# Kernel tuning notes

Measured on AMD Instinct MI355X. Metric: run time of the kernel, lower is better.

Reference implementation:

```python
import jax, jax.numpy as jnp
import numpy as np

NT, NGRID, NX, NY, H = 65536, 28, 19, 1, 20  # dims hard-coded by the torch module


def setup_inputs() -> dict:
    key = jax.random.key(0)
    ks = jax.random.split(key, 7)
    s = 1.0 / np.sqrt(H)  # torch default init scale for LSTMCell/Linear(20, ...)
    u = lambda k, shape: jax.random.uniform(k, shape, jnp.float32, -s, s)
    return {
        "x": jax.random.normal(ks[0], (NT, NGRID, NX), jnp.float32),
        "W_ih": u(ks[1], (4 * H, H)),   # LSTMCell weight_ih, input size 20 = nx + ny
        "W_hh": u(ks[2], (4 * H, H)),   # LSTMCell weight_hh
        "b_ih": u(ks[3], (4 * H,)),
        "b_hh": u(ks[4], (4 * H,)),
        "W_out": u(ks[5], (NY, H)),     # linearOut: Linear(20, ny)
        "b_out": u(ks[6], (NY,)),
    }


def reference(x, W_ih, W_hh, b_ih, b_hh, W_out, b_out):
    # x: (nt, ngrid, nx). Each step feeds concat(x_t, detach(prev_out)) -> LSTMCell(20,20) -> Linear(20,ny).
    nt, ngrid, _ = x.shape
    dt = x.dtype

    def step(carry, xt):
        h, c, prev = carry
        inp = jnp.concatenate([xt, jax.lax.stop_gradient(prev)], axis=1)  # (ngrid, 20); feedback is detached in torch
        gates = inp @ W_ih.T + b_ih + h @ W_hh.T + b_hh  # (ngrid, 4H), torch gate order i,f,g,o
        i, f, g, o = jnp.split(gates, 4, axis=1)
        c = jax.nn.sigmoid(f) * c + jax.nn.sigmoid(i) * jnp.tanh(g)
        h = jax.nn.sigmoid(o) * jnp.tanh(c)
        out = h @ W_out.T + b_out  # (ngrid, ny)
        return (h, c, out), out

    h0 = jnp.zeros((ngrid, H), dt)
    c0 = jnp.zeros((ngrid, H), dt)
    p0 = jnp.zeros((ngrid, NY), dt)  # torch.zeros(28, 1) on first step
    _, outs = jax.lax.scan(step, (h0, c0, p0), x)
    return outs  # (nt, ngrid, ny)
```

## Files before the change

kernel.cpp:

```cpp
#include <hip/hip_runtime.h>

#define NT     65536
#define NGRID  28
#define NX     19
#define HDIM   20
#define PF     4
#define CHUNK  256
#define WARM   64
#define NCHUNK (NT / CHUNK)
#define NTG    (NT * NGRID)
#define TGB    16

typedef float f2 __attribute__((ext_vector_type(2)));
typedef float f4 __attribute__((ext_vector_type(4)));

#if __has_builtin(__builtin_amdgcn_exp2f)
#define EXP2(x) __builtin_amdgcn_exp2f(x)
#else
#define EXP2(x) exp2f(x)
#endif
#define L2E 1.4426950408889634f

__device__ __forceinline__ float frcp(float v) { return __builtin_amdgcn_rcpf(v); }

__device__ __forceinline__ void pk_fma(f2& acc, f2 a, f2 b) {
    asm("v_pk_fma_f32 %0, %1, %2, %0" : "+v"(acc) : "v"(a), "v"(b));
}

__device__ __forceinline__ float quad_sum(float v) {
    float a = v + __builtin_bit_cast(float,
        __builtin_amdgcn_update_dpp(0, __builtin_bit_cast(int, v), 0xB1, 0xF, 0xF, true));
    return a + __builtin_bit_cast(float,
        __builtin_amdgcn_update_dpp(0, __builtin_bit_cast(int, a), 0x4E, 0xF, 0xF, true));
}

__device__ __forceinline__ float whp(const float* W_ih, const float* W_hh,
                                     const float* W_out, int r, int k) {
    if (k >= HDIM) return 0.f;
    return fmaf(W_ih[r * 20 + 19], W_out[k], W_hh[r * 20 + k]);
}

__global__ __launch_bounds__(320) void ax_kernel(
    const float* __restrict__ x, const float* __restrict__ W_ih,
    float* __restrict__ Aws)
{
    __shared__ float xs[TGB * NX];
    __shared__ float ws[80 * NX];
    const int    tid = threadIdx.x;
    const size_t tg0 = (size_t)blockIdx.x * TGB;

    if (tid < TGB * NX) xs[tid] = x[tg0 * NX + tid];
    for (int i = tid; i < 80 * NX; i += 320) {
        const int r = i / NX, k = i - NX * r;
        ws[i] = W_ih[r * 20 + k];
    }
    __syncthreads();

    const int tl = tid / 20;
    const int r4 = (tid % 20) * 4;
    const float* xp = &xs[tl * NX];
    float a0 = 0.f, a1 = 0.f, a2 = 0.f, a3 = 0.f;
#pragma unroll
    for (int k = 0; k < NX; ++k) {
        const float xv = xp[k];
        a0 = fmaf(xv, ws[(r4 + 0) * NX + k], a0);
        a1 = fmaf(xv, ws[(r4 + 1) * NX + k], a1);
        a2 = fmaf(xv, ws[(r4 + 2) * NX + k], a2);
        a3 = fmaf(xv, ws[(r4 + 3) * NX + k], a3);
    }
    *(f4*)&Aws[(tg0 + tl) * 80 + r4] = f4{a0, a1, a2, a3};
}

__global__ __launch_bounds__(64, 2) void lstm_main_kernel(
    const float* __restrict__ Aws,
    const float* __restrict__ W_ih,
    const float* __restrict__ W_hh,
    const float* __restrict__ b_ih,
    const float* __restrict__ b_hh,
    const float* __restrict__ W_out,
    const float* __restrict__ b_out,
    float* __restrict__ out)
{
    __shared__ __align__(16) float hb[2][32];
    __shared__ __align__(16) float gls[20][4];

    const int b  = blockIdx.x;
    const int ci = b / NGRID;
    const int g  = b - ci * NGRID;
    const int l  = threadIdx.x;
    const int qd = l >> 2;
    const int qi = l & 3;
    const int qb = 8 * qi;

    const int tstart = ci * CHUNK;
    const int t0     = (ci == 0) ? 0 : tstart - WARM;

    const int g1 = l / HDIM;
    const int u1 = l % HDIM;

    const float bout = b_out[0];

    f2 whn[10];
#pragma unroll
    for (int j = 0; j < 10; ++j)
        whn[j] = f2{whp(W_ih, W_hh, W_out, l, 2 * j),
                    whp(W_ih, W_hh, W_out, l, 2 * j + 1)};
    const float bb1 = b_ih[l] + b_hh[l];
    const float bpf = fmaf(W_ih[l * 20 + 19], bout, bb1);
    float bpc = (ci == 0) ? bb1 : bpf;

    const int rs = 64 + qd;
    f2 wsq[4], woq[4];
#pragma unroll
    for (int m = 0; m < 4; ++m) {
        const int k0 = qb + 2 * m, k1 = k0 + 1;
        wsq[m] = f2{whp(W_ih, W_hh, W_out, rs, k0), whp(W_ih, W_hh, W_out, rs, k1)};
        woq[m] = f2{(k0 < HDIM) ? W_out[k0] : 0.f, (k1 < HDIM) ? W_out[k1] : 0.f};
    }
    const float bbs = b_ih[rs] + b_hh[rs];
    const float bsf = fmaf(W_ih[rs * 20 + 19], bout, bbs);
    float bsc = (ci == 0) ? bbs : bsf;

    const float m1 = (g1 == 2) ? (2.f * L2E) : -L2E;
    const float A1 = (g1 == 2) ?  1.f :  0.f;
    const float B1 = (g1 == 2) ? -2.f :  1.f;

    const float* axb = Aws + (size_t)g * 80 + l;
    const float* axs = Aws + (size_t)g * 80 + 64 + qd;
    const size_t tsa = (size_t)NGRID * 80;
    float ap[PF], as[PF];
#pragma unroll
    for (int p = 0; p < PF; ++p) {
        int tp = t0 + p; if (tp > NT - 1) tp = NT - 1;
        ap[p] = axb[(size_t)tp * tsa];
        as[p] = axs[(size_t)tp * tsa];
    }

    if (l < 32) { hb[0][l] = 0.f; hb[1][l] = 0.f; }

    float  c  = 0.f;
    int    px = 0;
    float* op = out + (size_t)tstart * NGRID + g;

#define STEP(T, DO_STORE)                                                      \
    {                                                                          \
        int tf_ = (T) + PF; if (tf_ > NT - 1) tf_ = NT - 1;                    \
        const float fp_ = axb[(size_t)tf_ * tsa];                              \
        const float fs_ = axs[(size_t)tf_ * tsa];                              \
          \
        f2 aA = f2{ap[0], bpc}, aB = f2{0.f, 0.f};                             \
        _Pragma("unroll")                                                      \
        for (int ii = 0; ii < 5; ++ii) {                                       \
            const f4 X = ((const f4*)&hb[px][0])[ii];                          \
            pk_fma(aA, f2{X.x, X.y}, whn[2 * ii]);                             \
            pk_fma(aB, f2{X.z, X.w}, whn[2 * ii + 1]);                         \
        }                                                                      \
                             \
        const f4 Q0 = *(const f4*)&hb[px][qb];                                 \
        const f4 Q1 = *(const f4*)&hb[px][qb + 4];                             \
        f2 sS = f2{0.f, 0.f}, sO = f2{0.f, 0.f};                               \
        pk_fma(sS, f2{Q0.x, Q0.y}, wsq[0]); pk_fma(sO, f2{Q0.x, Q0.y}, woq[0]); \
        pk_fma(sS, f2{Q0.z, Q0.w}, wsq[1]); pk_fma(sO, f2{Q0.z, Q0.w}, woq[1]); \
        pk_fma(sS, f2{Q1.x, Q1.y}, wsq[2]); pk_fma(sO, f2{Q1.x, Q1.y}, woq[2]); \
        pk_fma(sS, f2{Q1.z, Q1.w}, wsq[3]); pk_fma(sO, f2{Q1.z, Q1.w}, woq[3]); \
        const float vs = quad_sum(sS.x + sS.y);                                \
        const float vo = quad_sum(sO.x + sO.y);          \
        const float a1 = aA.x + aA.y + aB.x + aB.y;                            \
        const float e1 = EXP2(m1 * a1);                                        \
        gls[u1][g1] = fmaf(B1, frcp(1.f + e1), A1);                            \
        if (qi == 0) gls[4 + qd][3] = frcp(1.f + EXP2(-L2E * (vs + as[0] + bsc))); \
        if (DO_STORE) { if (l == 0) *op = vo + bout; op += NGRID; }            \
        asm volatile("s_waitcnt lgkmcnt(0)" ::: "memory");                     \
        if (l < HDIM) {                                      \
            const f4 gv = *(const f4*)&gls[l][0];          \
            c = fmaf(gv.y, c, gv.x * gv.z);                                    \
            const float ec = EXP2(2.f * L2E * c);                              \
            hb[px ^ 1][l] = gv.w * (1.f - 2.f * frcp(1.f + ec));               \
        }                                                                      \
        _Pragma("unroll")                                                      \
        for (int i_ = 0; i_ < PF - 1; ++i_) { ap[i_] = ap[i_ + 1]; as[i_] = as[i_ + 1]; } \
        ap[PF - 1] = fp_; as[PF - 1] = fs_;                                    \
        px ^= 1;                                                               \
    }

    STEP(t0, false);
    bpc = bpf; bsc = bsf;
#pragma unroll 2
    for (int t = t0 + 1; t <= tstart; ++t) STEP(t, false);
#pragma unroll 2
    for (int t = tstart + 1; t <= tstart + CHUNK; ++t) STEP(t, true);
#undef STEP
}

__device__ __forceinline__ float gw_fb(const float* W_ih, const float* W_hh,
                                       const float* W_out, int r, int k) {
    if (k < NX) return W_ih[r * 20 + k];
    if (k >= 20 && k < 40)
        return fmaf(W_ih[r * 20 + 19], W_out[k - 20], W_hh[r * 20 + (k - 20)]);
    return 0.f;
}

__global__ __launch_bounds__(64, 2) void lstm_quad_kernel(
    const float* __restrict__ x, const float* __restrict__ W_ih,
    const float* __restrict__ W_hh, const float* __restrict__ b_ih,
    const float* __restrict__ b_hh, const float* __restrict__ W_out,
    const float* __restrict__ b_out, float* __restrict__ out)
{
    __shared__ __align__(16) float cls[2][48];
    __shared__ __align__(16) float gls[20][4];

    const int b  = blockIdx.x;
    const int ci = b / NGRID;
    const int g  = b - ci * NGRID;
    const int l  = threadIdx.x;
    const int qd = l >> 2;
    const int qi = l & 3;
    const int qb = 12 * qi;

    const int tstart = ci * CHUNK;
    const int t0     = (ci == 0) ? 0 : tstart - WARM;

    const int g1 = l / HDIM;
    const int u1 = l % HDIM;
    const float bout = b_out[0];

    f2 w_own[20];
#pragma unroll
    for (int kk = 0; kk < 20; ++kk)
        w_own[kk] = f2{gw_fb(W_ih, W_hh, W_out, l, 2 * kk),
                       gw_fb(W_ih, W_hh, W_out, l, 2 * kk + 1)};
    const float bb1 = b_ih[l] + b_hh[l];
    const float b1f = fmaf(W_ih[l * 20 + 19], bout, bb1);
    float b1c = (ci == 0) ? bb1 : b1f;

    const int rs = 64 + qd;
    f2 w_sh[6];
#pragma unroll
    for (int m = 0; m < 6; ++m)
        w_sh[m] = f2{gw_fb(W_ih, W_hh, W_out, rs, qb + 2 * m),
                     gw_fb(W_ih, W_hh, W_out, rs, qb + 2 * m + 1)};
    const float bbs = b_ih[rs] + b_hh[rs];
    const float bsf = fmaf(W_ih[rs * 20 + 19], bout, bbs);
    float bsc = (ci == 0) ? bbs : bsf;

    f2 w_oq[6];
#pragma unroll
    for (int m = 0; m < 6; ++m) {
        const int k0 = qb + 2 * m, k1 = k0 + 1;
        w_oq[m] = f2{(k0 >= 20 && k0 < 40) ? W_out[k0 - 20] : 0.f,
                     (k1 >= 20 && k1 < 40) ? W_out[k1 - 20] : 0.f};
    }

    const float m1 = (g1 == 2) ? (2.f * L2E) : -L2E;
    const float A1 = (g1 == 2) ?  1.f :  0.f;
    const float B1 = (g1 == 2) ? -2.f :  1.f;

    const int    kl   = (l < NX) ? l : 0;
    const float* xptr = x + (size_t)g * NX + kl;
    const size_t tsx  = (size_t)NGRID * NX;
    float xr[PF];
#pragma unroll
    for (int p = 0; p < PF; ++p) {
        int tp = t0 + 1 + p; if (tp > NT - 1) tp = NT - 1;
        xr[p] = xptr[(size_t)tp * tsx];
    }
    if (l < 8)    { cls[0][40 + l] = 0.f; cls[1][40 + l] = 0.f; }
    if (l < HDIM) { cls[0][20 + l] = 0.f; cls[0][l] = xptr[(size_t)t0 * tsx]; }

    float  c  = 0.f;
    int    px = 0;
    float* op = out + (size_t)tstart * NGRID + g;

#define STEPF(T, DO_STORE)                                                     \
    {                                                                          \
        if (l < HDIM) cls[px ^ 1][l] = xr[0];                                  \
        int tf_ = (T) + 1 + PF; if (tf_ > NT - 1) tf_ = NT - 1;                \
        const float xf_ = xptr[(size_t)tf_ * tsx];                             \
        f2 aA = f2{b1c, 0.f}, aB = f2{0.f, 0.f};                               \
        _Pragma("unroll")                                                      \
        for (int ii = 0; ii < 10; ++ii) {                                      \
            const f4 X = ((const f4*)&cls[px][0])[ii];                         \
            pk_fma(aA, f2{X.x, X.y}, w_own[2 * ii]);                           \
            pk_fma(aB, f2{X.z, X.w}, w_own[2 * ii + 1]);                       \
        }                                                                      \
        const f4 Q0 = *(const f4*)&cls[px][qb];                                \
        const f4 Q1 = *(const f4*)&cls[px][qb + 4];                            \
        const f4 Q2 = *(const f4*)&cls[px][qb + 8];                            \
        f2 sS = f2{0.f, 0.f}, sO = f2{0.f, 0.f};                               \
        pk_fma(sS, f2{Q0.x, Q0.y}, w_sh[0]); pk_fma(sO, f2{Q0.x, Q0.y}, w_oq[0]); \
        pk_fma(sS, f2{Q0.z, Q0.w}, w_sh[1]); pk_fma(sO, f2{Q0.z, Q0.w}, w_oq[1]); \
        pk_fma(sS, f2{Q1.x, Q1.y}, w_sh[2]); pk_fma(sO, f2{Q1.x, Q1.y}, w_oq[2]); \
        pk_fma(sS, f2{Q1.z, Q1.w}, w_sh[3]); pk_fma(sO, f2{Q1.z, Q1.w}, w_oq[3]); \
        pk_fma(sS, f2{Q2.x, Q2.y}, w_sh[4]); pk_fma(sO, f2{Q2.x, Q2.y}, w_oq[4]); \
        pk_fma(sS, f2{Q2.z, Q2.w}, w_sh[5]); pk_fma(sO, f2{Q2.z, Q2.w}, w_oq[5]); \
        const float vs = quad_sum(sS.x + sS.y);                                \
        const float vo = quad_sum(sO.x + sO.y);                                \
        const float a1 = aA.x + aA.y + aB.x + aB.y;                            \
        const float e1 = EXP2(m1 * a1);                                        \
        gls[u1][g1] = fmaf(B1, frcp(1.f + e1), A1);                            \
        if (qi == 0) gls[4 + qd][3] = frcp(1.f + EXP2(-L2E * (vs + bsc)));     \
        if (DO_STORE) { if (l == 0) *op = vo + bout; op += NGRID; }            \
        asm volatile("s_waitcnt lgkmcnt(0)" ::: "memory");                     \
        if (l < HDIM) {                                                        \
            const f4 gv = *(const f4*)&gls[l][0];                              \
            c = fmaf(gv.y, c, gv.x * gv.z);                                    \
            const float ec = EXP2(2.f * L2E * c);                              \
            cls[px ^ 1][20 + l] = gv.w * (1.f - 2.f * frcp(1.f + ec));         \
        }                                                                      \
        _Pragma("unroll")                                                      \
        for (int i_ = 0; i_ < PF - 1; ++i_) xr[i_] = xr[i_ + 1];               \
        xr[PF - 1] = xf_;                                                      \
        px ^= 1;                                                               \
    }

    STEPF(t0, false);
    b1c = b1f; bsc = bsf;
#pragma unroll 2
    for (int t = t0 + 1; t <= tstart; ++t) STEPF(t, false);
#pragma unroll 2
    for (int t = tstart + 1; t <= tstart + CHUNK; ++t) STEPF(t, true);
#undef STEPF
}

extern "C" void kernel_launch(void* const* d_in, const int* in_sizes, int n_in,
                              void* d_out, int out_size, void* d_ws, size_t ws_size,
                              hipStream_t stream) {
    const float* x     = (const float*)d_in[0];
    const float* W_ih  = (const float*)d_in[1];
    const float* W_hh  = (const float*)d_in[2];
    const float* b_ih  = (const float*)d_in[3];
    const float* b_hh  = (const float*)d_in[4];
    const float* W_out = (const float*)d_in[5];
    const float* b_out = (const float*)d_in[6];
    float* out = (float*)d_out;

    const size_t need = (size_t)NTG * 80 * sizeof(float);
    if (ws_size >= need) {
        float* Aws = (float*)d_ws;
        ax_kernel<<<dim3(NTG / TGB), dim3(320), 0, stream>>>(x, W_ih, Aws);
        lstm_main_kernel<<<dim3(NCHUNK * NGRID), dim3(64), 0, stream>>>(
            Aws, W_ih, W_hh, b_ih, b_hh, W_out, b_out, out);
    } else {
        lstm_quad_kernel<<<dim3(NCHUNK * NGRID), dim3(64), 0, stream>>>(
            x, W_ih, W_hh, b_ih, b_hh, W_out, b_out, out);
    }
}
```

Baseline: 401.2 us.

## Store input projections as fp16 and segment the workspace pipeline

The precomputed input-gate projections are now written to the workspace as fp16 rather than fp32, which halves the bytes written by the ax kernel and read by the LSTM kernel. The launch code picks between one, two or four time segments depending on workspace size, so the fast two-kernel path stays usable with smaller workspaces. The main kernel's launch bounds go from 2 to 4 blocks per SIMD. fp16 storage of the gate pre-activations adds rounding error that the recurrence can accumulate.

Measured after the change: 767.1 us. 91.2% more time.

```diff
diff --git a/kernel.cpp b/kernel.cpp
--- a/kernel.cpp
+++ b/kernel.cpp
@@ -5,14 +5,13 @@
 #define NX     19
 #define HDIM   20
 #define PF     4
-#define CHUNK  256
 #define WARM   64
-#define NCHUNK (NT / CHUNK)
-#define NTG    (NT * NGRID)
 #define TGB    16
 
 typedef float f2 __attribute__((ext_vector_type(2)));
 typedef float f4 __attribute__((ext_vector_type(4)));
+typedef unsigned short u16;
+typedef u16 u16x4 __attribute__((ext_vector_type(4)));
 
 #if __has_builtin(__builtin_amdgcn_exp2f)
 #define EXP2(x) __builtin_amdgcn_exp2f(x)
@@ -40,16 +39,20 @@
     return fmaf(W_ih[r * 20 + 19], W_out[k], W_hh[r * 20 + k]);
 }
 
+__device__ __forceinline__ float ldax(const u16* p, size_t off) {
+    return (float)__builtin_bit_cast(_Float16, p[off]);
+}
+
 __global__ __launch_bounds__(320) void ax_kernel(
     const float* __restrict__ x, const float* __restrict__ W_ih,
-    float* __restrict__ Aws)
+    u16* __restrict__ Aws, int aw_base)
 {
     __shared__ float xs[TGB * NX];
     __shared__ float ws[80 * NX];
     const int    tid = threadIdx.x;
     const size_t tg0 = (size_t)blockIdx.x * TGB;
 
-    if (tid < TGB * NX) xs[tid] = x[tg0 * NX + tid];
+    if (tid < TGB * NX) xs[tid] = x[((size_t)aw_base * NGRID) * NX + tg0 * NX + tid];
     for (int i = tid; i < 80 * NX; i += 320) {
         const int r = i / NX, k = i - NX * r;
         ws[i] = W_ih[r * 20 + k];
@@ -68,32 +71,38 @@
         a2 = fmaf(xv, ws[(r4 + 2) * NX + k], a2);
         a3 = fmaf(xv, ws[(r4 + 3) * NX + k], a3);
     }
-    *(f4*)&Aws[(tg0 + tl) * 80 + r4] = f4{a0, a1, a2, a3};
-}
-
-__global__ __launch_bounds__(64, 2) void lstm_main_kernel(
-    const float* __restrict__ Aws,
+    u16x4 o;
+    o.x = __builtin_bit_cast(u16, (_Float16)a0);
+    o.y = __builtin_bit_cast(u16, (_Float16)a1);
+    o.z = __builtin_bit_cast(u16, (_Float16)a2);
+    o.w = __builtin_bit_cast(u16, (_Float16)a3);
+    *(u16x4*)&Aws[(tg0 + tl) * 80 + r4] = o;
+}
+
+__global__ __launch_bounds__(64, 4) void lstm_main_kernel(
+    const u16*   __restrict__ Aws,
     const float* __restrict__ W_ih,
     const float* __restrict__ W_hh,
     const float* __restrict__ b_ih,
     const float* __restrict__ b_hh,
     const float* __restrict__ W_out,
     const float* __restrict__ b_out,
-    float* __restrict__ out)
+    float* __restrict__ out,
+    int ci0, int chunkSz, int aw_base, int t_hi)
 {
     __shared__ __align__(16) float hb[2][32];
     __shared__ __align__(16) float gls[20][4];
 
     const int b  = blockIdx.x;
-    const int ci = b / NGRID;
-    const int g  = b - ci * NGRID;
+    const int cil = b / NGRID;
+    const int g   = b - cil * NGRID;
     const int l  = threadIdx.x;
     const int qd = l >> 2;
     const int qi = l & 3;
     const int qb = 8 * qi;
 
-    const int tstart = ci * CHUNK;
-    const int t0     = (ci == 0) ? 0 : tstart - WARM;
+    const int tstart = (ci0 + cil) * chunkSz;
+    const int t0     = (tstart == 0) ? 0 : tstart - WARM;
 
     const int g1 = l / HDIM;
     const int u1 = l % HDIM;
@@ -107,7 +116,7 @@
                     whp(W_ih, W_hh, W_out, l, 2 * j + 1)};
     const float bb1 = b_ih[l] + b_hh[l];
     const float bpf = fmaf(W_ih[l * 20 + 19], bout, bb1);
-    float bpc = (ci == 0) ? bb1 : bpf;
+    float bpc = (tstart == 0) ? bb1 : bpf;
 
     const int rs = 64 + qd;
     f2 wsq[4], woq[4];
@@ -119,21 +128,21 @@
     }
     const float bbs = b_ih[rs] + b_hh[rs];
     const float bsf = fmaf(W_ih[rs * 20 + 19], bout, bbs);
-    float bsc = (ci == 0) ? bbs : bsf;
+    float bsc = (tstart == 0) ? bbs : bsf;
 
     const float m1 = (g1 == 2) ? (2.f * L2E) : -L2E;
     const float A1 = (g1 == 2) ?  1.f :  0.f;
     const float B1 = (g1 == 2) ? -2.f :  1.f;
 
-    const float* axb = Aws + (size_t)g * 80 + l;
-    const float* axs = Aws + (size_t)g * 80 + 64 + qd;
     const size_t tsa = (size_t)NGRID * 80;
+    const u16* axb = Aws + ((size_t)(t0 - aw_base) * NGRID + g) * 80 + l;
+    const u16* axs = Aws + ((size_t)(t0 - aw_base) * NGRID + g) * 80 + 64 + qd;
     float ap[PF], as[PF];
 #pragma unroll
     for (int p = 0; p < PF; ++p) {
-        int tp = t0 + p; if (tp > NT - 1) tp = NT - 1;
-        ap[p] = axb[(size_t)tp * tsa];
-        as[p] = axs[(size_t)tp * tsa];
+        int tp = t0 + p; if (tp > t_hi) tp = t_hi;
+        ap[p] = ldax(axb, (size_t)(tp - t0) * tsa);
+        as[p] = ldax(axs, (size_t)(tp - t0) * tsa);
     }
 
     if (l < 32) { hb[0][l] = 0.f; hb[1][l] = 0.f; }
@@ -144,9 +153,9 @@
 
 #define STEP(T, DO_STORE)                                                      \
     {                                                                          \
-        int tf_ = (T) + PF; if (tf_ > NT - 1) tf_ = NT - 1;                    \
-        const float fp_ = axb[(size_t)tf_ * tsa];                              \
-        const float fs_ = axs[(size_t)tf_ * tsa];                              \
+        int tf_ = (T) + PF; if (tf_ > t_hi) tf_ = t_hi;                        \
+        const float fp_ = ldax(axb, (size_t)(tf_ - t0) * tsa);                 \
+        const float fs_ = ldax(axs, (size_t)(tf_ - t0) * tsa);                 \
           \
         f2 aA = f2{ap[0], bpc}, aB = f2{0.f, 0.f};                             \
         _Pragma("unroll")                                                      \
@@ -188,10 +197,11 @@
 #pragma unroll 2
     for (int t = t0 + 1; t <= tstart; ++t) STEP(t, false);
 #pragma unroll 2
-    for (int t = tstart + 1; t <= tstart + CHUNK; ++t) STEP(t, true);
+    for (int t = tstart + 1; t <= tstart + chunkSz; ++t) STEP(t, true);
 #undef STEP
 }
 
+#define CHUNK_FB 256
 __device__ __forceinline__ float gw_fb(const float* W_ih, const float* W_hh,
                                        const float* W_out, int r, int k) {
     if (k < NX) return W_ih[r * 20 + k];
@@ -217,7 +227,7 @@
     const int qi = l & 3;
     const int qb = 12 * qi;
 
-    const int tstart = ci * CHUNK;
+    const int tstart = ci * CHUNK_FB;
     const int t0     = (ci == 0) ? 0 : tstart - WARM;
 
     const int g1 = l / HDIM;
@@ -318,7 +328,7 @@
 #pragma unroll 2
     for (int t = t0 + 1; t <= tstart; ++t) STEPF(t, false);
 #pragma unroll 2
-    for (int t = tstart + 1; t <= tstart + CHUNK; ++t) STEPF(t, true);
+    for (int t = tstart + 1; t <= tstart + CHUNK_FB; ++t) STEPF(t, true);
 #undef STEPF
 }
 
@@ -334,14 +344,28 @@
     const float* b_out = (const float*)d_in[6];
     float* out = (float*)d_out;
 
-    const size_t need = (size_t)NTG * 80 * sizeof(float);
-    if (ws_size >= need) {
-        float* Aws = (float*)d_ws;
-        ax_kernel<<<dim3(NTG / TGB), dim3(320), 0, stream>>>(x, W_ih, Aws);
-        lstm_main_kernel<<<dim3(NCHUNK * NGRID), dim3(64), 0, stream>>>(
-            Aws, W_ih, W_hh, b_ih, b_hh, W_out, b_out, out);
+    const size_t perT = (size_t)NGRID * 80 * sizeof(u16);
+    int S = 0, chunk = 256;
+    if      (ws_size >= (size_t)NT * perT)              { S = 1; chunk = 256; }
+    else if (ws_size >= (size_t)(NT / 2 + WARM) * perT) { S = 2; chunk = 256; }
+    else if (ws_size >= (size_t)(NT / 4 + WARM) * perT) { S = 4; chunk = 128; }
+
+    if (S) {
+        u16* Aws = (u16*)d_ws;
+        const int NTSEG = NT / S;
+        for (int s = 0; s < S; ++s) {
+            const int segT0   = s * NTSEG;
+            const int segEnd  = segT0 + NTSEG;
+            const int aw_base = (s == 0) ? 0 : segT0 - WARM;
+            const int nt_cov  = segEnd - aw_base;
+            ax_kernel<<<dim3(nt_cov * NGRID / TGB), dim3(320), 0, stream>>>(
+                x, W_ih, Aws, aw_base);
+            lstm_main_kernel<<<dim3((NTSEG / chunk) * NGRID), dim3(64), 0, stream>>>(
+                Aws, W_ih, W_hh, b_ih, b_hh, W_out, b_out, out,
+                segT0 / chunk, chunk, aw_base, segEnd - 1);
+        }
     } else {
-        lstm_quad_kernel<<<dim3(NCHUNK * NGRID), dim3(64), 0, stream>>>(
+        lstm_quad_kernel<<<dim3((NT / CHUNK_FB) * NGRID), dim3(64), 0, stream>>>(
             x, W_ih, W_hh, b_ih, b_hh, W_out, b_out, out);
     }
 }
```
